# Optimization experiments

Hardware: AMD Instinct MI355X
Metric: run time of the kernel (lower is better)

## Reference

```python
import jax, jax.numpy as jnp
import numpy as np

B, S, D = 4, 2048, 1024  # batch, seq_len, input_dimension
KD, VD = 1024, 1024      # key_dim, value_dim


def setup_inputs() -> dict:
    key = jax.random.key(0)
    ks = jax.random.split(key, 9)
    sc_in = 1.0 / np.sqrt(D)
    sc_v = 1.0 / np.sqrt(VD)
    return {
        "x":  jax.random.normal(ks[0], (B, S, D), dtype=jnp.float32),
        "Wq": jax.random.normal(ks[1], (KD, D), dtype=jnp.float32) * sc_in,
        "bq": jax.random.normal(ks[2], (KD,), dtype=jnp.float32) * 0.01,
        "Wk": jax.random.normal(ks[3], (KD, D), dtype=jnp.float32) * sc_in,
        "bk": jax.random.normal(ks[4], (KD,), dtype=jnp.float32) * 0.01,
        "Wv": jax.random.normal(ks[5], (VD, D), dtype=jnp.float32) * sc_in,
        "bv": jax.random.normal(ks[6], (VD,), dtype=jnp.float32) * 0.01,
        "Wo": jax.random.normal(ks[7], (D, VD), dtype=jnp.float32) * sc_v,
        "bo": jax.random.normal(ks[8], (D,), dtype=jnp.float32) * 0.01,
    }


def reference(x, Wq, bq, Wk, bk, Wv, bv, Wo, bo):
    # projections (torch Linear: x @ W.T + b)
    q = jnp.einsum('bsd,kd->bsk', x, Wq) + bq   # (B,S,KD)
    k = jnp.einsum('bsd,kd->bsk', x, Wk) + bk   # (B,S,KD)
    v = jnp.einsum('bsd,vd->bsv', x, Wv) + bv   # (B,S,VD)

    scores = jnp.einsum('bqk,bsk->bqs', q, k) / jnp.sqrt(jnp.float32(KD))  # (B,S,S)

    # sign rescale: scores * sign(scores) (sign(0) mapped to 1) == |scores| with zeros kept
    sign_mask = jnp.sign(scores)
    sign_mask = sign_mask + (sign_mask == 0).astype(jnp.float32)

    # causal mask: lower-triangular (incl diag) multiplied by 1, strict upper -> -inf
    seq = scores.shape[-1]
    causal = jnp.tril(jnp.ones((seq, seq), dtype=bool))
    masked = jnp.where(causal, scores * sign_mask, -jnp.inf)

    weights = jax.nn.softmax(masked, axis=2)            # (B,S,S)
    out = jnp.einsum('bqs,bsv->bqv', weights, v)        # (B,S,VD)
    return jnp.einsum('bqv,dv->bqd', out, Wo) + bo      # (B,S,D)
```

## Files before the change

kernel.cpp:

```cpp
#include <hip/hip_runtime.h>
#include <hip/hip_bf16.h>
#include <cstdint>


#define BM 128

typedef __attribute__((ext_vector_type(8))) __bf16 bf16x8;
typedef __attribute__((ext_vector_type(4))) __bf16 bf16x4;
typedef __attribute__((ext_vector_type(4))) float floatx4;

struct Ptr3 { const float* p[3]; };

__device__ __forceinline__ void async_copy16(const __bf16* g, const __bf16* l) {
  __builtin_amdgcn_global_load_lds(
      (const __attribute__((address_space(1))) unsigned int*)(const void*)g,
      (__attribute__((address_space(3))) unsigned int*)(unsigned)(uintptr_t)(const void*)l,
      16, 0, 0);
}

__device__ __forceinline__ void gemm_core(const __bf16* __restrict__ pA,
                                          const __bf16* __restrict__ pB,
                                          int K, int kBeg, int kEnd, int mb,
                                          int nb, floatx4 (&acc)[4][4]) {
  __shared__ __align__(16) __bf16 As[3][BM * 32];
  __shared__ __align__(16) __bf16 Bs[3][BM * 32];

  const int t = threadIdx.x;
  const int lane = t & 63;
  const int wave = t >> 6;
  const int quad = lane >> 4;
  const int l16 = lane & 15;
  const int wm = wave >> 1;
  const int wn = wave & 1;
  const int qsw = quad ^ ((l16 >> 1) & 3);

  const int srow = t >> 2;
  const int scol = ((t & 3) ^ ((t >> 3) & 3)) * 8;
  const __bf16* gA = pA + (long)(mb * BM + srow) * K + scol;
  const __bf16* gB = pB + (long)(nb * BM + srow) * K + scol;
  const long rowHalf = (long)64 * K;

  auto stage = [&](int kk, int buf) {
    const long ko = (long)kk * 32;
    __bf16* lA = &As[buf][t * 8];
    __bf16* lB = &Bs[buf][t * 8];
    async_copy16(gA + ko, lA);
    async_copy16(gA + ko + rowHalf, lA + 2048);
    async_copy16(gB + ko, lB);
    async_copy16(gB + ko + rowHalf, lB + 2048);
  };

  stage(kBeg, 0);
  stage(kBeg + 1 < kEnd ? kBeg + 1 : kEnd - 1, 1);

  for (int kk = kBeg; kk < kEnd; ++kk) {
    const int cur = (kk - kBeg) % 3;
    asm volatile("s_waitcnt vmcnt(4)" ::: "memory");
    __builtin_amdgcn_s_barrier();
    __builtin_amdgcn_sched_barrier(0);
    {
      const int nxt = kk + 2;
      stage(nxt < kEnd ? nxt : kEnd - 1, (cur + 2) % 3);
    }
    const __bf16* Asp = &As[cur][0];
    const __bf16* Bsp = &Bs[cur][0];
    bf16x8 af[4], bfr[4];
#pragma unroll
    for (int i = 0; i < 4; ++i) {
      af[i] = *(const bf16x8*)&Asp[(wm * 64 + i * 16 + l16) * 32 + qsw * 8];
      bfr[i] = *(const bf16x8*)&Bsp[(wn * 64 + i * 16 + l16) * 32 + qsw * 8];
    }
#pragma unroll
    for (int i = 0; i < 4; ++i)
#pragma unroll
      for (int j = 0; j < 4; ++j)
        acc[i][j] = __builtin_amdgcn_mfma_f32_16x16x32_bf16(af[i], bfr[j],
                                                            acc[i][j], 0, 0, 0);
  }
  __syncthreads();
}

__global__ void prep2(const float* __restrict__ Wo, Ptr3 tp,
                      const float* __restrict__ bv, const float* __restrict__ bq,
                      const float* __restrict__ bk,
                      __bf16* __restrict__ Wob, __bf16* __restrict__ Wqt,
                      __bf16* __restrict__ Wkt, __bf16* __restrict__ Wvt,
                      float* __restrict__ bvo, float* __restrict__ cscal,
                      float* __restrict__ lsum) {
  __shared__ __bf16 tile[64][66];
  __shared__ float wsum[4];
  const int bid = blockIdx.x;
  const int t = threadIdx.x;
  if (bid < 1024) {
    const long e = ((long)bid * 256 + t) * 4;
    const float4 f = *(const float4*)(Wo + e);
    bf16x4 o;
    o[0] = (__bf16)f.x; o[1] = (__bf16)f.y; o[2] = (__bf16)f.z; o[3] = (__bf16)f.w;
    *(bf16x4*)(Wob + e) = o;
  } else if (bid < 1792) {
    const int seg = (bid - 1024) >> 8;
    const int idx = (bid - 1024) & 255;
    const float* src = tp.p[seg];
    __bf16* dstw = seg == 0 ? Wqt : (seg == 1 ? Wkt : Wvt);
    const int r0 = (idx >> 4) * 64, c0 = (idx & 15) * 64;
#pragma unroll
    for (int e = 0; e < 16; ++e) {
      const int i = e * 256 + t;
      const int r = i >> 6, c = i & 63;
      tile[r][c] = (__bf16)src[(long)(r0 + r) * 1024 + (c0 + c)];
    }
    __syncthreads();
#pragma unroll
    for (int e = 0; e < 16; ++e) {
      const int i = e * 256 + t;
      const int r = i >> 6, c = i & 63;
      dstw[(long)(c0 + r) * 1024 + (r0 + c)] = tile[c][r];
    }
  } else if (bid < 2816) {
    const int d = bid - 1792;
    const float* row = Wo + (long)d * 1024;
    float s = 0.f;
    for (int v = t; v < 1024; v += 256) s += bv[v] * row[v];
#pragma unroll
    for (int off = 32; off > 0; off >>= 1) s += __shfl_down(s, off, 64);
    if ((t & 63) == 0) wsum[t >> 6] = s;
    __syncthreads();
    if (t == 0) bvo[d] = wsum[0] + wsum[1] + wsum[2] + wsum[3];
  } else if (bid == 2816) {
    float s = 0.f;
    for (int i = t; i < 1024; i += 256) s += bq[i] * bk[i];
#pragma unroll
    for (int off = 32; off > 0; off >>= 1) s += __shfl_down(s, off, 64);
    if ((t & 63) == 0) wsum[t >> 6] = s;
    __syncthreads();
    if (t == 0) *cscal = wsum[0] + wsum[1] + wsum[2] + wsum[3];
  } else {
#pragma unroll
    for (int e = 0; e < 8; ++e)
      *(float4*)(lsum + (e * 256 + t) * 4) = float4{0.f, 0.f, 0.f, 0.f};
  }
}

__global__ void __launch_bounds__(256, 3)
gemmA(const __bf16* __restrict__ Wkt, const __bf16* __restrict__ Wqt,
      const __bf16* __restrict__ Wob, const __bf16* __restrict__ Wvt,
      __bf16* __restrict__ Mt, __bf16* __restrict__ Wvo,
      const float* __restrict__ bk, const float* __restrict__ bq,
      float* __restrict__ m1f, float* __restrict__ m2f,
      const float* __restrict__ x, __bf16* __restrict__ xb) {
  const int id = blockIdx.x;
  const int t = threadIdx.x;

  if (id >= 160) {
    const long i = ((long)(id - 160) * 256 + t) * 4;
    const float4 f = *(const float4*)(x + i);
    bf16x4 o;
    o[0] = (__bf16)f.x; o[1] = (__bf16)f.y; o[2] = (__bf16)f.z; o[3] = (__bf16)f.w;
    *(bf16x4*)(xb + i) = o;
    return;
  }
  if (id >= 128) {
    const int q = (id - 128) & 15;
    const bool isM2 = (id - 128) >= 16;
    const __bf16* Wt = isM2 ? Wkt : Wqt;
    const float* bvec = isM2 ? bq : bk;
    float* dst = isM2 ? m2f : m1f;
    const int lane = t & 63, wave = t >> 6, qd = lane >> 4, l16 = lane & 15;
#pragma unroll
    for (int rr = 0; rr < 4; ++rr) {
      const int row = q * 64 + (wave * 4 + qd) * 4 + rr;
      const __bf16* wr = Wt + (long)row * 1024 + l16 * 64;
      const float* bp = bvec + l16 * 64;
      float s = 0.f;
#pragma unroll
      for (int jj = 0; jj < 8; ++jj) {
        bf16x8 wv = *(const bf16x8*)(wr + jj * 8);
#pragma unroll
        for (int e = 0; e < 8; ++e) s += (float)wv[e] * bp[jj * 8 + e];
      }
      s += __shfl_xor(s, 1, 64);
      s += __shfl_xor(s, 2, 64);
      s += __shfl_xor(s, 4, 64);
      s += __shfl_xor(s, 8, 64);
      if (l16 == 0) dst[row] = s;
    }
    return;
  }

  const __bf16 *pA, *pB;
  __bf16* dst;
  int mb, nb;
  if (id < 64) {
    mb = id >> 3; nb = id & 7;
    pA = Wkt; pB = Wqt; dst = Mt;
  } else {
    const int w = id - 64;
    mb = w >> 3; nb = w & 7;
    pA = Wob; pB = Wvt; dst = Wvo;
  }

  floatx4 acc[4][4] = {};
  gemm_core(pA, pB, 1024, 0, 32, mb, nb, acc);

  const int lane = t & 63, wave = t >> 6;
  const int rb = (wave >> 1) * 64 + (lane >> 4) * 4;
  const int cb = (wave & 1) * 64 + (lane & 15);
#pragma unroll
  for (int j4 = 0; j4 < 4; ++j4) {
    const int gc = nb * 128 + cb + j4 * 16;
#pragma unroll
    for (int i = 0; i < 4; ++i) {
      const int gr = mb * BM + rb + i * 16;
#pragma unroll
      for (int r = 0; r < 4; ++r)
        dst[(long)(gr + r) * 1024 + gc] = (__bf16)acc[i][j4][r];
    }
  }
}

__global__ void __launch_bounds__(256, 3)
gemmB1(const __bf16* __restrict__ xb, const __bf16* __restrict__ Mt,
       const float* __restrict__ m2f, __bf16* __restrict__ y2,
       const float* __restrict__ m1f, const float* __restrict__ cscal,
       float* __restrict__ uvec) {
  const int id = blockIdx.x;
  const int t = threadIdx.x;

  if (id >= 512) {
    const int k = id - 512;
    const int lane = t & 63, wave = t >> 6, qd = lane >> 4, l16 = lane & 15;
    const float c = *cscal;
#pragma unroll
    for (int rr = 0; rr < 4; ++rr) {
      const int row = k * 64 + (wave * 4 + qd) * 4 + rr;
      const __bf16* xr = xb + (long)row * 1024 + l16 * 64;
      const float* mp = m1f + l16 * 64;
      float s = 0.f;
#pragma unroll
      for (int jj = 0; jj < 8; ++jj) {
        bf16x8 xv = *(const bf16x8*)(xr + jj * 8);
#pragma unroll
        for (int e = 0; e < 8; ++e) s += (float)xv[e] * mp[jj * 8 + e];
      }
      s += __shfl_xor(s, 1, 64);
      s += __shfl_xor(s, 2, 64);
      s += __shfl_xor(s, 4, 64);
      s += __shfl_xor(s, 8, 64);
      if (l16 == 0) uvec[row] = s + c;
    }
    return;
  }

  const int xcd = id & 7;
  const int j = id >> 3;
  const int mb = xcd * 8 + (j & 7);
  const int nb = j >> 3;

  floatx4 acc[4][4] = {};
  gemm_core(xb, Mt, 1024, 0, 32, mb, nb, acc);

  const int lane = t & 63, wave = t >> 6;
  const int rb = (wave >> 1) * 64 + (lane >> 4) * 4;
  const int cb = (wave & 1) * 64 + (lane & 15);
#pragma unroll
  for (int j4 = 0; j4 < 4; ++j4) {
    const int gc = nb * 128 + cb + j4 * 16;
    const float bvv = m2f[gc];
#pragma unroll
    for (int i = 0; i < 4; ++i) {
      const int gr = mb * BM + rb + i * 16;
#pragma unroll
      for (int r = 0; r < 4; ++r)
        y2[(long)(gr + r) * 1024 + gc] = (__bf16)(acc[i][j4][r] + bvv);
    }
  }
}

__global__ void __launch_bounds__(256, 3)
gemmB2(const __bf16* __restrict__ xb, const __bf16* __restrict__ Wvo,
       const float* __restrict__ bvo, __bf16* __restrict__ Ut,
       const __bf16* __restrict__ y2, const float* __restrict__ uvec,
       __bf16* __restrict__ P, float* __restrict__ lsum,
       int S, int KD, int D) {
  const int id = blockIdx.x;
  const __bf16 *pA, *pB;
  int mb, nb, b, mode;
  if (id < 512) {
    const int xcd = id & 7;
    const int j = id >> 3;
    mb = xcd * 8 + (j & 7);
    nb = j >> 3;
    b = 0;
    mode = 0;
    pA = xb;
    pB = Wvo;
  } else {
    const int sid = id - 512;
    const int xcd = sid & 7;
    const int r = sid >> 3;
    b = r / 17;
    const int ci = r - b * 17;
    const int n1 = xcd + 1;
    mb = (ci < n1) ? xcd : (15 - xcd);
    nb = (ci < n1) ? ci : (ci - n1);
    mode = 1;
    pA = y2 + (long)b * S * KD;
    pB = xb + (long)b * S * KD;
  }

  floatx4 acc[4][4] = {};
  gemm_core(pA, pB, KD, 0, KD / 32, mb, nb, acc);

  const int t = threadIdx.x;
  const int lane = t & 63, wave = t >> 6;
  const int l16 = lane & 15;
  const int rb = (wave >> 1) * 64 + (lane >> 4) * 4;
  const int cb = (wave & 1) * 64 + l16;

  if (mode == 0) {
    const int bb = (mb * BM) / S;
    const int s0 = mb * BM - bb * S;
#pragma unroll
    for (int j4 = 0; j4 < 4; ++j4) {
      const int gc = nb * 128 + cb + j4 * 16;
      const float bv = bvo[gc];
#pragma unroll
      for (int i = 0; i < 4; ++i) {
        const int sr = s0 + rb + i * 16;
        bf16x4 o;
#pragma unroll
        for (int r = 0; r < 4; ++r) o[r] = (__bf16)(acc[i][j4][r] + bv);
        *(bf16x4*)&Ut[((long)bb * D + gc) * S + sr] = o;
      }
    }
  } else {
    __bf16* C = P + (long)b * S * S;
    float* lrow = lsum + (long)b * S;
    const float sc = 0.03125f;
#pragma unroll
    for (int i = 0; i < 4; ++i) {
#pragma unroll
      for (int r = 0; r < 4; ++r) {
        const int row = mb * BM + rb + i * 16 + r;
        const float urow = uvec[(long)b * S + row];
        float psum = 0.f;
#pragma unroll
        for (int j4 = 0; j4 < 4; ++j4) {
          const int col = nb * 128 + cb + j4 * 16;
          const float p =
              (col <= row) ? __expf(fabsf(acc[i][j4][r] + urow) * sc) : 0.f;
          psum += p;
          C[(long)row * S + col] = (__bf16)p;
        }
        psum += __shfl_xor(psum, 1, 64);
        psum += __shfl_xor(psum, 2, 64);
        psum += __shfl_xor(psum, 4, 64);
        psum += __shfl_xor(psum, 8, 64);
        if (l16 == 0) atomicAdd(&lrow[row], psum);
      }
    }
  }
}

__global__ void __launch_bounds__(256, 3)
gemm_pvo(const __bf16* __restrict__ P, const __bf16* __restrict__ Ut,
         const float* __restrict__ lsum, const float* __restrict__ bo,
         float* __restrict__ out, int S, int D) {
  const int id = blockIdx.x;
  const int xcd = id & 7;
  const int j = id >> 3;
  const int half = j >> 5;
  const int idx = j & 31;
  const int b = idx >> 3;
  const int nb = idx & 7;
  const int mb = half ? xcd : (15 - xcd);

  floatx4 acc[4][4] = {};
  gemm_core(P + (long)b * S * S, Ut + (long)b * D * S, S, 0, 4 * (mb + 1), mb,
            nb, acc);

  const int t = threadIdx.x;
  const int lane = t & 63, wave = t >> 6;
  const int rb = (wave >> 1) * 64 + (lane >> 4) * 4;
  const int cb = (wave & 1) * 64 + (lane & 15);
  const float* lrow = lsum + (long)b * S;

#pragma unroll
  for (int i = 0; i < 4; ++i) {
#pragma unroll
    for (int r = 0; r < 4; ++r) {
      const int row = mb * BM + rb + i * 16 + r;
      const float inv = 1.f / lrow[row];
#pragma unroll
      for (int j4 = 0; j4 < 4; ++j4) {
        const int col = nb * 128 + cb + j4 * 16;
        out[((long)b * S + row) * D + col] = acc[i][j4][r] * inv + bo[col];
      }
    }
  }
}

extern "C" void kernel_launch(void* const* d_in, const int* in_sizes, int n_in,
                              void* d_out, int out_size, void* d_ws, size_t ws_size,
                              hipStream_t stream) {
  const float* x = (const float*)d_in[0];
  const float* Wq = (const float*)d_in[1];
  const float* bq = (const float*)d_in[2];
  const float* Wk = (const float*)d_in[3];
  const float* bk = (const float*)d_in[4];
  const float* Wv = (const float*)d_in[5];
  const float* bv = (const float*)d_in[6];
  const float* Wo = (const float*)d_in[7];
  const float* bo = (const float*)d_in[8];
  float* out = (float*)d_out;

  constexpr int B = 4, S = 2048, D = 1024, KD = 1024;
  constexpr long MB_ = 1024 * 1024;

  char* w = (char*)d_ws;
  __bf16* xb  = (__bf16*)(w);
  __bf16* y2  = (__bf16*)(w + 16 * MB_);
  __bf16* Ut  = (__bf16*)(w + 32 * MB_);
  __bf16* P   = (__bf16*)(w + 48 * MB_);
  __bf16* Wob = (__bf16*)(w + 80 * MB_);
  __bf16* Wqt = (__bf16*)(w + 82 * MB_);
  __bf16* Wkt = (__bf16*)(w + 84 * MB_);
  __bf16* Wvt = (__bf16*)(w + 86 * MB_);
  __bf16* Mt  = (__bf16*)(w + 88 * MB_);
  __bf16* Wvo = (__bf16*)(w + 90 * MB_);
  float* lsum  = (float*)(w + 92 * MB_);
  float* uvec  = (float*)(w + 92 * MB_ + 32768);
  float* bvo   = (float*)(w + 92 * MB_ + 65536);
  float* m2f   = (float*)(w + 92 * MB_ + 69632);
  float* m1f   = (float*)(w + 92 * MB_ + 73728);
  float* cscal = (float*)(w + 92 * MB_ + 77824);

  Ptr3 tp{{Wq, Wk, Wv}};
  prep2<<<2818, 256, 0, stream>>>(Wo, tp, bv, bq, bk, Wob, Wqt, Wkt, Wvt,
                                  bvo, cscal, lsum);

  gemmA<<<8352, 256, 0, stream>>>(Wkt, Wqt, Wob, Wvt, Mt, Wvo, bk, bq,
                                  m1f, m2f, x, xb);

  gemmB1<<<640, 256, 0, stream>>>(xb, Mt, m2f, y2, m1f, cscal, uvec);

  gemmB2<<<1056, 256, 0, stream>>>(xb, Wvo, bvo, Ut, y2, uvec, P, lsum, S, KD, D);

  gemm_pvo<<<512, 256, 0, stream>>>(P, Ut, lsum, bo, out, S, D);
}
```

Measured before the change: 237.0 us.

## Merge y2 and value projection GEMMs into one 256x256-tile kernel

Adds a 256x256-tile GEMM core with 512-thread blocks. The two x-by-matrix GEMMs (y2 = x·M and Ut = x·Wvo) now run in a single launch instead of being split across two kernels, and the uvec row-dot work moves into the same launch. The scores GEMM gets its own kernel. Larger tiles are meant to raise arithmetic intensity and cut global/LDS traffic per FLOP. The cost is fewer blocks (256 GEMM blocks), which may underfill the CUs, and higher register and LDS pressure.

```diff
diff --git a/kernel.cpp b/kernel.cpp
--- a/kernel.cpp
+++ b/kernel.cpp
@@ -72,6 +72,69 @@
     }
 #pragma unroll
     for (int i = 0; i < 4; ++i)
+#pragma unroll
+      for (int j = 0; j < 4; ++j)
+        acc[i][j] = __builtin_amdgcn_mfma_f32_16x16x32_bf16(af[i], bfr[j],
+                                                            acc[i][j], 0, 0, 0);
+  }
+  __syncthreads();
+}
+
+__device__ __forceinline__ void gemm_core256(const __bf16* __restrict__ pA,
+                                             const __bf16* __restrict__ pB,
+                                             int K, int kBeg, int kEnd, int mb,
+                                             int nb, floatx4 (&acc)[8][4]) {
+  __shared__ __align__(16) __bf16 As[3][256 * 32];
+  __shared__ __align__(16) __bf16 Bs[3][256 * 32];
+
+  const int t = threadIdx.x;
+  const int lane = t & 63;
+  const int wave = t >> 6;
+  const int quad = lane >> 4;
+  const int l16 = lane & 15;
+  const int wm = wave >> 2;
+  const int wn = wave & 3;
+  const int qsw = quad ^ ((l16 >> 1) & 3);
+
+  const int srow = t >> 2;
+  const int scol = ((t & 3) ^ ((t >> 3) & 3)) * 8;
+  const __bf16* gA = pA + (long)(mb * 256 + srow) * K + scol;
+  const __bf16* gB = pB + (long)(nb * 256 + srow) * K + scol;
+  const long rowHalf = (long)128 * K;
+
+  auto stage = [&](int kk, int buf) {
+    const long ko = (long)kk * 32;
+    __bf16* lA = &As[buf][t * 8];
+    __bf16* lB = &Bs[buf][t * 8];
+    async_copy16(gA + ko, lA);
+    async_copy16(gA + ko + rowHalf, lA + 4096);
+    async_copy16(gB + ko, lB);
+    async_copy16(gB + ko + rowHalf, lB + 4096);
+  };
+
+  stage(kBeg, 0);
+  stage(kBeg + 1 < kEnd ? kBeg + 1 : kEnd - 1, 1);
+
+  for (int kk = kBeg; kk < kEnd; ++kk) {
+    const int cur = (kk - kBeg) % 3;
+    asm volatile("s_waitcnt vmcnt(4)" ::: "memory");
+    __builtin_amdgcn_s_barrier();
+    __builtin_amdgcn_sched_barrier(0);
+    {
+      const int nxt = kk + 2;
+      stage(nxt < kEnd ? nxt : kEnd - 1, (cur + 2) % 3);
+    }
+    const __bf16* Asp = &As[cur][0];
+    const __bf16* Bsp = &Bs[cur][0];
+    bf16x8 af[8], bfr[4];
+#pragma unroll
+    for (int j = 0; j < 4; ++j)
+      bfr[j] = *(const bf16x8*)&Bsp[(wn * 64 + j * 16 + l16) * 32 + qsw * 8];
+#pragma unroll
+    for (int i = 0; i < 8; ++i)
+      af[i] = *(const bf16x8*)&Asp[(wm * 128 + i * 16 + l16) * 32 + qsw * 8];
+#pragma unroll
+    for (int i = 0; i < 8; ++i)
 #pragma unroll
       for (int j = 0; j < 4; ++j)
         acc[i][j] = __builtin_amdgcn_mfma_f32_16x16x32_bf16(af[i], bfr[j],
@@ -218,95 +281,96 @@
   }
 }
 
+__global__ void __launch_bounds__(512, 2)
+big1(const __bf16* __restrict__ xb, const __bf16* __restrict__ Mt,
+     const __bf16* __restrict__ Wvo, const float* __restrict__ m2f,
+     const float* __restrict__ bvo, __bf16* __restrict__ y2,
+     __bf16* __restrict__ Ut, const float* __restrict__ m1f,
+     const float* __restrict__ cscal, float* __restrict__ uvec,
+     int S, int D) {
+  const int id = blockIdx.x;
+  const int t = threadIdx.x;
+
+  if (id >= 256) {
+    const int k = id - 256;
+    const int row = k * 64 + (t >> 3);
+    const int l8 = t & 7;
+    const float c = *cscal;
+    const __bf16* xr = xb + (long)row * 1024 + l8 * 128;
+    const float* mp = m1f + l8 * 128;
+    float s = 0.f;
+#pragma unroll
+    for (int jj = 0; jj < 16; ++jj) {
+      bf16x8 xv = *(const bf16x8*)(xr + jj * 8);
+#pragma unroll
+      for (int e = 0; e < 8; ++e) s += (float)xv[e] * mp[jj * 8 + e];
+    }
+    s += __shfl_xor(s, 1, 64);
+    s += __shfl_xor(s, 2, 64);
+    s += __shfl_xor(s, 4, 64);
+    if (l8 == 0) uvec[row] = s + c;
+    return;
+  }
+
+  const bool isY2 = id < 128;
+  const int w = isY2 ? id : id - 128;
+  const int mb = w >> 2;
+  const int nb = w & 3;
+  const __bf16* pB = isY2 ? Mt : Wvo;
+
+  floatx4 acc[8][4] = {};
+  gemm_core256(xb, pB, 1024, 0, 32, mb, nb, acc);
+
+  const int lane = t & 63, wave = t >> 6;
+  const int quad = lane >> 4, l16 = lane & 15;
+  const int wm = wave >> 2, wn = wave & 3;
+
+  if (isY2) {
+#pragma unroll
+    for (int j = 0; j < 4; ++j) {
+      const int gc = nb * 256 + wn * 64 + j * 16 + l16;
+      const float bvv = m2f[gc];
+#pragma unroll
+      for (int i = 0; i < 8; ++i) {
+        const int gr = mb * 256 + wm * 128 + i * 16 + quad * 4;
+#pragma unroll
+        for (int r = 0; r < 4; ++r)
+          y2[(long)(gr + r) * 1024 + gc] = (__bf16)(acc[i][j][r] + bvv);
+      }
+    }
+  } else {
+    const int bb = (mb * 256) / S;
+    const int s0 = mb * 256 - bb * S;
+#pragma unroll
+    for (int j = 0; j < 4; ++j) {
+      const int gc = nb * 256 + wn * 64 + j * 16 + l16;
+      const float bv = bvo[gc];
+#pragma unroll
+      for (int i = 0; i < 8; ++i) {
+        const int sr = s0 + wm * 128 + i * 16 + quad * 4;
+        bf16x4 o;
+#pragma unroll
+        for (int r = 0; r < 4; ++r) o[r] = (__bf16)(acc[i][j][r] + bv);
+        *(bf16x4*)&Ut[((long)bb * D + gc) * S + sr] = o;
+      }
+    }
+  }
+}
+
 __global__ void __launch_bounds__(256, 3)
-gemmB1(const __bf16* __restrict__ xb, const __bf16* __restrict__ Mt,
-       const float* __restrict__ m2f, __bf16* __restrict__ y2,
-       const float* __restrict__ m1f, const float* __restrict__ cscal,
-       float* __restrict__ uvec) {
-  const int id = blockIdx.x;
-  const int t = threadIdx.x;
-
-  if (id >= 512) {
-    const int k = id - 512;
-    const int lane = t & 63, wave = t >> 6, qd = lane >> 4, l16 = lane & 15;
-    const float c = *cscal;
-#pragma unroll
-    for (int rr = 0; rr < 4; ++rr) {
-      const int row = k * 64 + (wave * 4 + qd) * 4 + rr;
-      const __bf16* xr = xb + (long)row * 1024 + l16 * 64;
-      const float* mp = m1f + l16 * 64;
-      float s = 0.f;
-#pragma unroll
-      for (int jj = 0; jj < 8; ++jj) {
-        bf16x8 xv = *(const bf16x8*)(xr + jj * 8);
-#pragma unroll
-        for (int e = 0; e < 8; ++e) s += (float)xv[e] * mp[jj * 8 + e];
-      }
-      s += __shfl_xor(s, 1, 64);
-      s += __shfl_xor(s, 2, 64);
-      s += __shfl_xor(s, 4, 64);
-      s += __shfl_xor(s, 8, 64);
-      if (l16 == 0) uvec[row] = s + c;
-    }
-    return;
-  }
-
-  const int xcd = id & 7;
-  const int j = id >> 3;
-  const int mb = xcd * 8 + (j & 7);
-  const int nb = j >> 3;
-
-  floatx4 acc[4][4] = {};
-  gemm_core(xb, Mt, 1024, 0, 32, mb, nb, acc);
-
-  const int lane = t & 63, wave = t >> 6;
-  const int rb = (wave >> 1) * 64 + (lane >> 4) * 4;
-  const int cb = (wave & 1) * 64 + (lane & 15);
-#pragma unroll
-  for (int j4 = 0; j4 < 4; ++j4) {
-    const int gc = nb * 128 + cb + j4 * 16;
-    const float bvv = m2f[gc];
-#pragma unroll
-    for (int i = 0; i < 4; ++i) {
-      const int gr = mb * BM + rb + i * 16;
-#pragma unroll
-      for (int r = 0; r < 4; ++r)
-        y2[(long)(gr + r) * 1024 + gc] = (__bf16)(acc[i][j4][r] + bvv);
-    }
-  }
-}
-
-__global__ void __launch_bounds__(256, 3)
-gemmB2(const __bf16* __restrict__ xb, const __bf16* __restrict__ Wvo,
-       const float* __restrict__ bvo, __bf16* __restrict__ Ut,
-       const __bf16* __restrict__ y2, const float* __restrict__ uvec,
-       __bf16* __restrict__ P, float* __restrict__ lsum,
-       int S, int KD, int D) {
-  const int id = blockIdx.x;
-  const __bf16 *pA, *pB;
-  int mb, nb, b, mode;
-  if (id < 512) {
-    const int xcd = id & 7;
-    const int j = id >> 3;
-    mb = xcd * 8 + (j & 7);
-    nb = j >> 3;
-    b = 0;
-    mode = 0;
-    pA = xb;
-    pB = Wvo;
-  } else {
-    const int sid = id - 512;
-    const int xcd = sid & 7;
-    const int r = sid >> 3;
-    b = r / 17;
-    const int ci = r - b * 17;
-    const int n1 = xcd + 1;
-    mb = (ci < n1) ? xcd : (15 - xcd);
-    nb = (ci < n1) ? ci : (ci - n1);
-    mode = 1;
-    pA = y2 + (long)b * S * KD;
-    pB = xb + (long)b * S * KD;
-  }
+scoresK(const __bf16* __restrict__ xb, const __bf16* __restrict__ y2,
+        const float* __restrict__ uvec, __bf16* __restrict__ P,
+        float* __restrict__ lsum, int S, int KD) {
+  const int sid = blockIdx.x;
+  const int xcd = sid & 7;
+  const int r = sid >> 3;
+  const int b = r / 17;
+  const int ci = r - b * 17;
+  const int n1 = xcd + 1;
+  const int mb = (ci < n1) ? xcd : (15 - xcd);
+  const int nb = (ci < n1) ? ci : (ci - n1);
+  const __bf16* pA = y2 + (long)b * S * KD;
+  const __bf16* pB = xb + (long)b * S * KD;
 
   floatx4 acc[4][4] = {};
   gemm_core(pA, pB, KD, 0, KD / 32, mb, nb, acc);
@@ -317,47 +381,29 @@
   const int rb = (wave >> 1) * 64 + (lane >> 4) * 4;
   const int cb = (wave & 1) * 64 + l16;
 
-  if (mode == 0) {
-    const int bb = (mb * BM) / S;
-    const int s0 = mb * BM - bb * S;
-#pragma unroll
-    for (int j4 = 0; j4 < 4; ++j4) {
-      const int gc = nb * 128 + cb + j4 * 16;
-      const float bv = bvo[gc];
-#pragma unroll
-      for (int i = 0; i < 4; ++i) {
-        const int sr = s0 + rb + i * 16;
-        bf16x4 o;
-#pragma unroll
-        for (int r = 0; r < 4; ++r) o[r] = (__bf16)(acc[i][j4][r] + bv);
-        *(bf16x4*)&Ut[((long)bb * D + gc) * S + sr] = o;
+  __bf16* C = P + (long)b * S * S;
+  float* lrow = lsum + (long)b * S;
+  const float sc = 0.03125f;
+#pragma unroll
+  for (int i = 0; i < 4; ++i) {
+#pragma unroll
+    for (int r4 = 0; r4 < 4; ++r4) {
+      const int row = mb * BM + rb + i * 16 + r4;
+      const float urow = uvec[(long)b * S + row];
+      float psum = 0.f;
+#pragma unroll
+      for (int j4 = 0; j4 < 4; ++j4) {
+        const int col = nb * 128 + cb + j4 * 16;
+        const float p =
+            (col <= row) ? __expf(fabsf(acc[i][j4][r4] + urow) * sc) : 0.f;
+        psum += p;
+        C[(long)row * S + col] = (__bf16)p;
       }
-    }
-  } else {
-    __bf16* C = P + (long)b * S * S;
-    float* lrow = lsum + (long)b * S;
-    const float sc = 0.03125f;
-#pragma unroll
-    for (int i = 0; i < 4; ++i) {
-#pragma unroll
-      for (int r = 0; r < 4; ++r) {
-        const int row = mb * BM + rb + i * 16 + r;
-        const float urow = uvec[(long)b * S + row];
-        float psum = 0.f;
-#pragma unroll
-        for (int j4 = 0; j4 < 4; ++j4) {
-          const int col = nb * 128 + cb + j4 * 16;
-          const float p =
-              (col <= row) ? __expf(fabsf(acc[i][j4][r] + urow) * sc) : 0.f;
-          psum += p;
-          C[(long)row * S + col] = (__bf16)p;
-        }
-        psum += __shfl_xor(psum, 1, 64);
-        psum += __shfl_xor(psum, 2, 64);
-        psum += __shfl_xor(psum, 4, 64);
-        psum += __shfl_xor(psum, 8, 64);
-        if (l16 == 0) atomicAdd(&lrow[row], psum);
-      }
+      psum += __shfl_xor(psum, 1, 64);
+      psum += __shfl_xor(psum, 2, 64);
+      psum += __shfl_xor(psum, 4, 64);
+      psum += __shfl_xor(psum, 8, 64);
+      if (l16 == 0) atomicAdd(&lrow[row], psum);
     }
   }
 }
@@ -442,9 +488,10 @@
   gemmA<<<8352, 256, 0, stream>>>(Wkt, Wqt, Wob, Wvt, Mt, Wvo, bk, bq,
                                   m1f, m2f, x, xb);
 
-  gemmB1<<<640, 256, 0, stream>>>(xb, Mt, m2f, y2, m1f, cscal, uvec);
-
-  gemmB2<<<1056, 256, 0, stream>>>(xb, Wvo, bvo, Ut, y2, uvec, P, lsum, S, KD, D);
+  big1<<<384, 512, 0, stream>>>(xb, Mt, Wvo, m2f, bvo, y2, Ut, m1f, cscal,
+                                uvec, S, D);
+
+  scoresK<<<544, 256, 0, stream>>>(xb, y2, uvec, P, lsum, S, KD);
 
   gemm_pvo<<<512, 256, 0, stream>>>(P, Ut, lsum, bo, out, S, D);
 }
```

Result: no change. 232.5 us (-1.9%).
